# Optimization experiments

Hardware: AMD Instinct MI355X
Metric: run time of the kernel (lower is better)

## Reference

```python
import jax, jax.numpy as jnp
import numpy as np

N = 100000      # nodes
E = 800000      # edges
F_IN = 128      # input feature dim
HID = 8         # per-head hidden
HEADS = 8
HD = HID * HEADS  # 64
G = 128         # graphs in batch
C = 10          # classes
SLOPE = 0.2     # leaky relu negative slope


def setup_inputs() -> dict:
    key = jax.random.key(0)
    ks = iter(jax.random.split(key, 48))
    def rn(shape, scale=0.1):
        return jax.random.normal(next(ks), shape, jnp.float32) * scale
    inp = {
        'x': jax.random.normal(next(ks), (N, F_IN), jnp.float32),
        'edge_index': jax.random.randint(next(ks), (2, E), 0, N),
        'batch': jnp.sort(jax.random.randint(next(ks), (N,), 0, G)),
        # GAT layer 1
        'W1': rn((F_IN, HEADS * HID)), 'as1': rn((HEADS, HID)), 'ad1': rn((HEADS, HID)), 'b1': jnp.zeros((HEADS * HID,), jnp.float32),
        # GAT layer 2
        'W2': rn((HD, HEADS * HID)), 'as2': rn((HEADS, HID)), 'ad2': rn((HEADS, HID)), 'b2': jnp.zeros((HEADS * HID,), jnp.float32),
        # node attention MLP (HD -> HD//2 -> 2)
        'na_w1': rn((HD, HD // 2)), 'na_b1': jnp.zeros((HD // 2,), jnp.float32), 'na_w2': rn((HD // 2, 2)), 'na_b2': jnp.zeros((2,), jnp.float32),
        # edge attention MLP (2*HD -> HD -> 2)
        'ea_w1': rn((2 * HD, HD)), 'ea_b1': jnp.zeros((HD,), jnp.float32), 'ea_w2': rn((HD, 2)), 'ea_b2': jnp.zeros((2,), jnp.float32),
        # GCN causal / trivial
        'gc_w': rn((HD, HD)), 'gc_b': jnp.zeros((HD,), jnp.float32),
        'gt_w': rn((HD, HD)), 'gt_b': jnp.zeros((HD,), jnp.float32),
        # readouts
        'rc_w': rn((HD, HD)), 'rc_b': jnp.zeros((HD,), jnp.float32),
        'rt_w': rn((HD, HD)), 'rt_b': jnp.zeros((HD,), jnp.float32),
        # classifiers (HD -> HD//2 -> C), combined (2HD -> HD -> C)
        'cc_w1': rn((HD, HD // 2)), 'cc_b1': jnp.zeros((HD // 2,), jnp.float32), 'cc_w2': rn((HD // 2, C)), 'cc_b2': jnp.zeros((C,), jnp.float32),
        'ct_w1': rn((HD, HD // 2)), 'ct_b1': jnp.zeros((HD // 2,), jnp.float32), 'ct_w2': rn((HD // 2, C)), 'ct_b2': jnp.zeros((C,), jnp.float32),
        'cm_w1': rn((2 * HD, HD)), 'cm_b1': jnp.zeros((HD,), jnp.float32), 'cm_w2': rn((HD, C)), 'cm_b2': jnp.zeros((C,), jnp.float32),
    }
    return inp


def _mlp2(h, w1, b1, w2, b2):
    return jax.nn.relu(h @ w1 + b1) @ w2 + b2


def reference(x, edge_index, batch,
              W1, as1, ad1, b1, W2, as2, ad2, b2,
              na_w1, na_b1, na_w2, na_b2,
              ea_w1, ea_b1, ea_w2, ea_b2,
              gc_w, gc_b, gt_w, gt_b,
              rc_w, rc_b, rt_w, rt_b,
              cc_w1, cc_b1, cc_w2, cc_b2,
              ct_w1, ct_b1, ct_w2, ct_b2,
              cm_w1, cm_b1, cm_w2, cm_b2):
    src, dst = edge_index[0], edge_index[1]
    loop = jnp.arange(N)
    s2 = jnp.concatenate([src, loop])  # edges + self-loops (PyG GATConv/GCNConv add self-loops)
    d2 = jnp.concatenate([dst, loop])

    def gat(h_in, W, a_s, a_d, b):
        h = (h_in @ W).reshape(N, HEADS, HID)
        es = jnp.einsum('nhd,hd->nh', h, a_s)
        ed = jnp.einsum('nhd,hd->nh', h, a_d)
        logit = jax.nn.leaky_relu(es[s2] + ed[d2], SLOPE)      # [E+N, H]
        m = jax.ops.segment_max(logit, d2, num_segments=N)
        ex = jnp.exp(logit - m[d2])
        den = jax.ops.segment_sum(ex, d2, num_segments=N)
        alpha = ex / (den[d2] + 1e-16)
        out = jax.ops.segment_sum(h[s2] * alpha[..., None], d2, num_segments=N)
        return out.reshape(N, HEADS * HID) + b

    # GNN encoder (dropout disabled: eval mode)
    H1 = jax.nn.elu(gat(x, W1, as1, ad1, b1))
    H = gat(H1, W2, as2, ad2, b2)                              # [N, HD]

    # node attention
    na = jax.nn.softmax(_mlp2(H, na_w1, na_b1, na_w2, na_b2), axis=1)
    alpha_c, alpha_t = na[:, 0], na[:, 1]
    # edge attention (original edges, no self-loops)
    ef = jnp.concatenate([H[src], H[dst]], axis=1)             # [E, 2*HD]
    ea = jax.nn.softmax(_mlp2(ef, ea_w1, ea_b1, ea_w2, ea_b2), axis=1)
    beta_c, beta_t = ea[:, 0], ea[:, 1]

    Hc = H * alpha_c[:, None]
    Ht = H * alpha_t[:, None]

    def gcn(h_in, w, b, ew):
        # PyG gcn_norm: self-loops with weight 1, symmetric deg^-1/2 normalization
        w_full = jnp.concatenate([ew, jnp.ones((N,), h_in.dtype)])
        deg = jax.ops.segment_sum(w_full, d2, num_segments=N)
        dis = jnp.where(deg > 0, jax.lax.rsqrt(jnp.maximum(deg, 1e-20)), 0.0)
        norm = dis[s2] * w_full * dis[d2]
        h = h_in @ w
        return jax.ops.segment_sum(h[s2] * norm[:, None], d2, num_segments=N) + b

    Gc = gcn(Hc, gc_w, gc_b, beta_c)
    Gt = gcn(Ht, gt_w, gt_b, beta_t)

    # readout: linear then global_add_pool
    hGc = jax.ops.segment_sum(Gc @ rc_w + rc_b, batch, num_segments=G)  # [G, HD]
    hGt = jax.ops.segment_sum(Gt @ rt_w + rt_b, batch, num_segments=G)

    zc = _mlp2(hGc, cc_w1, cc_b1, cc_w2, cc_b2)
    zt = _mlp2(hGt, ct_w1, ct_b1, ct_w2, ct_b2)
    # RandomIntervention: within-graph node shuffle followed by add-pool == plain add-pool
    h_comb = jnp.concatenate([hGc + hGt], axis=1) if False else (hGc + hGt)
    zp = _mlp2(jnp.concatenate([h_comb, jnp.zeros_like(h_comb)], axis=1), cm_w1, cm_b1, cm_w2, cm_b2) if False else _mlp2_comb(h_comb, cm_w1, cm_b1, cm_w2, cm_b2)
    return (zc, zt, zp, hGc, hGt)


def _mlp2_comb(h_comb, cm_w1, cm_b1, cm_w2, cm_b2):
    # original: classifier_combined takes hidden_dim*2 input; forward feeds h_G_c + shuffled_h_G_t
    # which is [G, HD]; to match Linear(2*HD, ...) we use the first HD rows of cm_w1 twice?
    # NO -- the original code as written passes a [G, HD] tensor to a Linear(2*HD, HD) layer,
    # which would error in torch. Faithful runnable interpretation: combined feature is
    # concat([h_G_c, shuffled_h_G_t]) of width 2*HD (the standard CAL formulation).
    return jax.nn.relu(h_comb @ cm_w1 + cm_b1) @ cm_w2 + cm_b2


# clean final definition overriding the commented exploration above
def reference(x, edge_index, batch,
              W1, as1, ad1, b1, W2, as2, ad2, b2,
              na_w1, na_b1, na_w2, na_b2,
              ea_w1, ea_b1, ea_w2, ea_b2,
              gc_w, gc_b, gt_w, gt_b,
              rc_w, rc_b, rt_w, rt_b,
              cc_w1, cc_b1, cc_w2, cc_b2,
              ct_w1, ct_b1, ct_w2, ct_b2,
              cm_w1, cm_b1, cm_w2, cm_b2):
    src, dst = edge_index[0], edge_index[1]
    loop = jnp.arange(N)
    s2 = jnp.concatenate([src, loop])
    d2 = jnp.concatenate([dst, loop])

    def gat(h_in, W, a_s, a_d, b):
        h = (h_in @ W).reshape(N, HEADS, HID)
        es = jnp.einsum('nhd,hd->nh', h, a_s)
        ed = jnp.einsum('nhd,hd->nh', h, a_d)
        logit = jax.nn.leaky_relu(es[s2] + ed[d2], SLOPE)
        m = jax.ops.segment_max(logit, d2, num_segments=N)
        ex = jnp.exp(logit - m[d2])
        den = jax.ops.segment_sum(ex, d2, num_segments=N)
        alpha = ex / (den[d2] + 1e-16)
        out = jax.ops.segment_sum(h[s2] * alpha[..., None], d2, num_segments=N)
        return out.reshape(N, HEADS * HID) + b

    H1 = jax.nn.elu(gat(x, W1, as1, ad1, b1))
    H = gat(H1, W2, as2, ad2, b2)

    na = jax.nn.softmax(_mlp2(H, na_w1, na_b1, na_w2, na_b2), axis=1)
    alpha_c, alpha_t = na[:, 0], na[:, 1]
    ef = jnp.concatenate([H[src], H[dst]], axis=1)
    ea = jax.nn.softmax(_mlp2(ef, ea_w1, ea_b1, ea_w2, ea_b2), axis=1)
    beta_c, beta_t = ea[:, 0], ea[:, 1]

    Hc = H * alpha_c[:, None]
    Ht = H * alpha_t[:, None]

    def gcn(h_in, w, b, ew):
        w_full = jnp.concatenate([ew, jnp.ones((N,), h_in.dtype)])
        deg = jax.ops.segment_sum(w_full, d2, num_segments=N)
        dis = jnp.where(deg > 0, jax.lax.rsqrt(jnp.maximum(deg, 1e-20)), 0.0)
        norm = dis[s2] * w_full * dis[d2]
        h = h_in @ w
        return jax.ops.segment_sum(h[s2] * norm[:, None], d2, num_segments=N) + b

    Gc = gcn(Hc, gc_w, gc_b, beta_c)
    Gt = gcn(Ht, gt_w, gt_b, beta_t)

    hGc = jax.ops.segment_sum(Gc @ rc_w + rc_b, batch, num_segments=G)
    hGt = jax.ops.segment_sum(Gt @ rt_w + rt_b, batch, num_segments=G)

    zc = _mlp2(hGc, cc_w1, cc_b1, cc_w2, cc_b2)
    zt = _mlp2(hGt, ct_w1, ct_b1, ct_w2, ct_b2)
    # RandomIntervention with sorted batch: within-graph permutation + add-pool == add-pool
    h_comb = jnp.concatenate([hGc, hGt], axis=1)  # [G, 2*HD] for Linear(2*HD, ...)
    zp = _mlp2(h_comb, cm_w1, cm_b1, cm_w2, cm_b2)
    return (zc, zt, zp, hGc, hGt)


if __name__ == '__main__':
    out = reference(**setup_inputs())
    print([o.shape for o in out])
```

## Files before the change

kernel.cpp:

```cpp
#include <hip/hip_runtime.h>
#include <hip/hip_bf16.h>

#define N_NODES 100000
#define E_EDGES 800000
#define E2 (E_EDGES + N_NODES)
#define FIN 128
#define HD 64
#define NH 8
#define NG 128
#define NC 10
#define SLOPE 0.2f
#define SELF_FLAG 0x40000000
#define SRC_MASK  0x3FFFFFFF
#define NSCAN_BLK 391
#define NBLK64 1563
#define GB 16

#define U1_STRIPES 261
#define U1_GRID (2 + U1_STRIPES * 7)
#define U1_HISTB (U1_STRIPES * 4)
#define T1 (U1_STRIPES * 3)
#define U2_STRIPES 391
#define U2_GRID (U2_STRIPES * 11)

typedef unsigned short bfu;

__device__ __forceinline__ float lrelu(float x) { return x > 0.f ? x : SLOPE * x; }

__device__ __forceinline__ bfu f2bf(float f) {
    unsigned int u = __float_as_uint(f);
    u += 0x7FFFu + ((u >> 16) & 1u);
    return (bfu)(u >> 16);
}
__device__ __forceinline__ float bf2f(bfu s) {
    return __uint_as_float(((unsigned int)s) << 16);
}
__device__ __forceinline__ float bflo(unsigned int u) { return __uint_as_float(u << 16); }
__device__ __forceinline__ float bfhi(unsigned int u) { return __uint_as_float(u & 0xFFFF0000u); }

template<typename TIN, int KIN, int MODE>
__device__ __forceinline__
void gemm_tile_body(float* smem, int tile,
                    const TIN* __restrict__ in, const float* __restrict__ W,
                    bfu* __restrict__ outB,
                    const float* __restrict__ a_s, const float* __restrict__ a_d,
                    float* __restrict__ es, float* __restrict__ ed)
{
    constexpr int KH = (KIN > 64) ? 64 : KIN;
    constexpr int RS = KIN + 4;
    float* Ws   = smem;
    float* rows = smem + KH * 64;
    int t = threadIdx.x;
    int base = tile * 64;

    if constexpr (sizeof(TIN) == 4) {
        constexpr int RQ = KIN / 4;
        for (int i = t; i < 64 * RQ; i += 256) {
            int r = i / RQ, c = (i % RQ) * 4;
            int n = base + r;
            float4 v = make_float4(0.f, 0.f, 0.f, 0.f);
            if (n < N_NODES) v = *(const float4*)((const float*)in + (size_t)n * KIN + c);
            *(float4*)(rows + r * RS + c) = v;
        }
    } else {
        constexpr int RQ = KIN / 8;
        for (int i = t; i < 64 * RQ; i += 256) {
            int r = i / RQ, c = (i % RQ) * 8;
            int n = base + r;
            uint4 v = make_uint4(0, 0, 0, 0);
            if (n < N_NODES) v = *(const uint4*)((const bfu*)in + (size_t)n * KIN + c);
            float* dp = rows + r * RS + c;
            *(float4*)dp       = make_float4(bflo(v.x), bfhi(v.x), bflo(v.y), bfhi(v.y));
            *(float4*)(dp + 4) = make_float4(bflo(v.z), bfhi(v.z), bflo(v.w), bfhi(v.w));
        }
    }

    int tr = t >> 4, tc = t & 15;
    float acc[4][4] = {};
    const float4* R4 = (const float4*)rows;

    for (int h = 0; h < KIN / KH; ++h) {
        __syncthreads();
        {
            const float4* Wv = (const float4*)(W + (size_t)h * KH * 64);
            float4* Wsv4 = (float4*)Ws;
            for (int i = t; i < KH * 16; i += 256) Wsv4[i] = Wv[i];
        }
        __syncthreads();
        const float4* Wsv = (const float4*)Ws;
#pragma unroll 2
        for (int k = 0; k < KH; k += 4) {
            float4 w0 = Wsv[(k + 0) * 16 + tc];
            float4 w1 = Wsv[(k + 1) * 16 + tc];
            float4 w2 = Wsv[(k + 2) * 16 + tc];
            float4 w3 = Wsv[(k + 3) * 16 + tc];
            int kq = (h * KH + k) >> 2;
#pragma unroll
            for (int i = 0; i < 4; ++i) {
                float4 r = R4[(tr * 4 + i) * (RS / 4) + kq];
                acc[i][0] = fmaf(r.x, w0.x, fmaf(r.y, w1.x, fmaf(r.z, w2.x, fmaf(r.w, w3.x, acc[i][0]))));
                acc[i][1] = fmaf(r.x, w0.y, fmaf(r.y, w1.y, fmaf(r.z, w2.y, fmaf(r.w, w3.y, acc[i][1]))));
                acc[i][2] = fmaf(r.x, w0.z, fmaf(r.y, w1.z, fmaf(r.z, w2.z, fmaf(r.w, w3.z, acc[i][2]))));
                acc[i][3] = fmaf(r.x, w0.w, fmaf(r.y, w1.w, fmaf(r.z, w2.w, fmaf(r.w, w3.w, acc[i][3]))));
            }
        }
    }

    int j0 = tc * 4;
#pragma unroll
    for (int i = 0; i < 4; ++i) {
        int n = base + tr * 4 + i;
        if (n < N_NODES) {
            ushort4 ov;
            ov.x = f2bf(acc[i][0]); ov.y = f2bf(acc[i][1]);
            ov.z = f2bf(acc[i][2]); ov.w = f2bf(acc[i][3]);
            *(ushort4*)(outB + (size_t)n * 64 + j0) = ov;
        }
    }
    if (MODE == 1) {
        float s0[4], s1[4];
#pragma unroll
        for (int i = 0; i < 4; ++i) {
            float pes = 0.f, ped = 0.f;
#pragma unroll
            for (int q = 0; q < 4; ++q) {
                pes = fmaf(acc[i][q], a_s[j0 + q], pes);
                ped = fmaf(acc[i][q], a_d[j0 + q], ped);
            }
            pes += __shfl_xor(pes, 1, 64);
            ped += __shfl_xor(ped, 1, 64);
            s0[i] = pes; s1[i] = ped;
        }
        if ((tc & 1) == 0) {
            int h = tc >> 1;
#pragma unroll
            for (int i = 0; i < 4; ++i) {
                int n = base + tr * 4 + i;
                if (n < N_NODES) {
                    es[n * NH + h] = s0[i];
                    ed[n * NH + h] = s1[i];
                }
            }
        }
    }
}

__device__ __forceinline__
void gemm_dual_body(float* smem, int tile,
                    const bfu* __restrict__ in, const float* __restrict__ W0,
                    const float* __restrict__ W1,
                    bfu* __restrict__ out0, bfu* __restrict__ out1)
{
    float* Ws   = smem;
    float* rows = smem + 8192;
    int t = threadIdx.x;
    int base = tile * 64;
    {
        const float4* W0v = (const float4*)W0;
        const float4* W1v = (const float4*)W1;
        float4* Wsv = (float4*)Ws;
        for (int i = t; i < 1024; i += 256) { Wsv[i] = W0v[i]; Wsv[1024 + i] = W1v[i]; }
    }
    for (int i = t; i < 64 * 8; i += 256) {
        int r = i >> 3, c = (i & 7) * 8;
        int n = base + r;
        uint4 v = make_uint4(0, 0, 0, 0);
        if (n < N_NODES) v = *(const uint4*)(in + (size_t)n * 64 + c);
        float* dp = rows + r * 68 + c;
        *(float4*)dp       = make_float4(bflo(v.x), bfhi(v.x), bflo(v.y), bfhi(v.y));
        *(float4*)(dp + 4) = make_float4(bflo(v.z), bfhi(v.z), bflo(v.w), bfhi(v.w));
    }
    __syncthreads();
    int tr = t >> 4, tc = t & 15;
    float a0[4][4] = {}, a1[4][4] = {};
    const float4* Wsv = (const float4*)Ws;
    const float4* R4 = (const float4*)rows;
#pragma unroll 2
    for (int k = 0; k < 64; k += 4) {
        float4 p0 = Wsv[(k + 0) * 16 + tc];
        float4 p1 = Wsv[(k + 1) * 16 + tc];
        float4 p2 = Wsv[(k + 2) * 16 + tc];
        float4 p3 = Wsv[(k + 3) * 16 + tc];
        float4 q0 = Wsv[1024 + (k + 0) * 16 + tc];
        float4 q1 = Wsv[1024 + (k + 1) * 16 + tc];
        float4 q2 = Wsv[1024 + (k + 2) * 16 + tc];
        float4 q3 = Wsv[1024 + (k + 3) * 16 + tc];
        int kq = k >> 2;
#pragma unroll
        for (int i = 0; i < 4; ++i) {
            float4 r = R4[(tr * 4 + i) * 17 + kq];
            a0[i][0] = fmaf(r.x, p0.x, fmaf(r.y, p1.x, fmaf(r.z, p2.x, fmaf(r.w, p3.x, a0[i][0]))));
            a0[i][1] = fmaf(r.x, p0.y, fmaf(r.y, p1.y, fmaf(r.z, p2.y, fmaf(r.w, p3.y, a0[i][1]))));
            a0[i][2] = fmaf(r.x, p0.z, fmaf(r.y, p1.z, fmaf(r.z, p2.z, fmaf(r.w, p3.z, a0[i][2]))));
            a0[i][3] = fmaf(r.x, p0.w, fmaf(r.y, p1.w, fmaf(r.z, p2.w, fmaf(r.w, p3.w, a0[i][3]))));
            a1[i][0] = fmaf(r.x, q0.x, fmaf(r.y, q1.x, fmaf(r.z, q2.x, fmaf(r.w, q3.x, a1[i][0]))));
            a1[i][1] = fmaf(r.x, q0.y, fmaf(r.y, q1.y, fmaf(r.z, q2.y, fmaf(r.w, q3.y, a1[i][1]))));
            a1[i][2] = fmaf(r.x, q0.z, fmaf(r.y, q1.z, fmaf(r.z, q2.z, fmaf(r.w, q3.z, a1[i][2]))));
            a1[i][3] = fmaf(r.x, q0.w, fmaf(r.y, q1.w, fmaf(r.z, q2.w, fmaf(r.w, q3.w, a1[i][3]))));
        }
    }
    int j0 = tc * 4;
#pragma unroll
    for (int i = 0; i < 4; ++i) {
        int n = base + tr * 4 + i;
        if (n >= N_NODES) continue;
        ushort4 o0, o1;
        o0.x = f2bf(a0[i][0]); o0.y = f2bf(a0[i][1]);
        o0.z = f2bf(a0[i][2]); o0.w = f2bf(a0[i][3]);
        o1.x = f2bf(a1[i][0]); o1.y = f2bf(a1[i][1]);
        o1.z = f2bf(a1[i][2]); o1.w = f2bf(a1[i][3]);
        *(ushort4*)(out0 + (size_t)n * 64 + j0) = o0;
        *(ushort4*)(out1 + (size_t)n * 64 + j0) = o1;
    }
}

__device__ __forceinline__
void node_att_body(float* smem, int tile,
                   const bfu* __restrict__ H, const float* __restrict__ w1,
                   const float* __restrict__ b1, const float* __restrict__ w2,
                   const float* __restrict__ b2, float2* __restrict__ al2)
{
    float* w1s  = smem;
    float* w2s  = smem + 2048;
    float* rows = smem + 2112;
    int t = threadIdx.x;
    int base = tile * 64;
    {
        const float4* w1v = (const float4*)w1;
        float4* dst = (float4*)w1s;
        for (int i = t; i < 512; i += 256) dst[i] = w1v[i];
    }
    if (t < 64) w2s[t] = w2[t];
    for (int i = t; i < 64 * 8; i += 256) {
        int r = i >> 3, c = (i & 7) * 8;
        int n = base + r;
        uint4 v = make_uint4(0, 0, 0, 0);
        if (n < N_NODES) v = *(const uint4*)(H + (size_t)n * 64 + c);
        float* dp = rows + r * 65 + c;
        dp[0] = bflo(v.x); dp[1] = bfhi(v.x);
        dp[2] = bflo(v.y); dp[3] = bfhi(v.y);
        dp[4] = bflo(v.z); dp[5] = bfhi(v.z);
        dp[6] = bflo(v.w); dp[7] = bfhi(v.w);
    }
    __syncthreads();
    int tr = t >> 3;
    int tc = t & 7;
    float4 bv = *(const float4*)(b1 + tc * 4);
    float4 acc0 = bv, acc1 = bv;
    const float4* w1sv = (const float4*)w1s;
#pragma unroll 8
    for (int k = 0; k < 64; ++k) {
        float4 w = w1sv[k * 8 + tc];
        float r0 = rows[tr * 65 + k];
        float r1 = rows[(tr + 32) * 65 + k];
        acc0.x = fmaf(r0, w.x, acc0.x); acc0.y = fmaf(r0, w.y, acc0.y);
        acc0.z = fmaf(r0, w.z, acc0.z); acc0.w = fmaf(r0, w.w, acc0.w);
        acc1.x = fmaf(r1, w.x, acc1.x); acc1.y = fmaf(r1, w.y, acc1.y);
        acc1.z = fmaf(r1, w.z, acc1.z); acc1.w = fmaf(r1, w.w, acc1.w);
    }
    float z00 = 0.f, z01 = 0.f, z10 = 0.f, z11 = 0.f;
    float h0, w20, w21;
    int j0 = tc * 4;
#pragma unroll
    for (int q = 0; q < 4; ++q) {
        float a0q = q == 0 ? acc0.x : q == 1 ? acc0.y : q == 2 ? acc0.z : acc0.w;
        float a1q = q == 0 ? acc1.x : q == 1 ? acc1.y : q == 2 ? acc1.z : acc1.w;
        w20 = w2s[(j0 + q) * 2]; w21 = w2s[(j0 + q) * 2 + 1];
        h0 = fmaxf(a0q, 0.f);
        z00 = fmaf(h0, w20, z00); z01 = fmaf(h0, w21, z01);
        h0 = fmaxf(a1q, 0.f);
        z10 = fmaf(h0, w20, z10); z11 = fmaf(h0, w21, z11);
    }
#pragma unroll
    for (int o = 1; o < 8; o <<= 1) {
        z00 += __shfl_xor(z00, o, 64); z01 += __shfl_xor(z01, o, 64);
        z10 += __shfl_xor(z10, o, 64); z11 += __shfl_xor(z11, o, 64);
    }
    if (tc == 0) {
        int n0 = base + tr, n1 = base + tr + 32;
        if (n0 < N_NODES) {
            float zz0 = z00 + b2[0], zz1 = z01 + b2[1];
            float mx = fmaxf(zz0, zz1);
            float e0 = __expf(zz0 - mx), e1 = __expf(zz1 - mx);
            float ss = e0 + e1;
            al2[n0] = make_float2(e0 / ss, e1 / ss);
        }
        if (n1 < N_NODES) {
            float zz0 = z10 + b2[0], zz1 = z11 + b2[1];
            float mx = fmaxf(zz0, zz1);
            float e0 = __expf(zz0 - mx), e1 = __expf(zz1 - mx);
            float ss = e0 + e1;
            al2[n1] = make_float2(e0 / ss, e1 / ss);
        }
    }
}

__device__ __forceinline__
void weight_prep_body(float* smem,
                      const float* __restrict__ gw, const float* __restrict__ gb,
                      const float* __restrict__ rw, const float* __restrict__ rb,
                      float* __restrict__ Wp, float* __restrict__ bp)
{
    float* A = smem;
    float* B = smem + 4096;
    int t = threadIdx.x;
    {
        const float4* ga = (const float4*)gw;
        const float4* rA = (const float4*)rw;
        float4* dA = (float4*)A; float4* dB = (float4*)B;
        for (int i = t; i < 1024; i += 256) { dA[i] = ga[i]; dB[i] = rA[i]; }
    }
    __syncthreads();
    for (int e = t * 16; e < t * 16 + 16; ++e) {
        int k = e >> 6, j = e & 63;
        float acc = 0.f;
#pragma unroll 8
        for (int m = 0; m < 64; ++m) acc = fmaf(A[k * 64 + m], B[m * 64 + j], acc);
        Wp[e] = acc;
    }
    if (t < 64) {
        float acc = rb[t];
#pragma unroll 8
        for (int m = 0; m < 64; ++m) acc = fmaf(gb[m], B[m * 64 + t], acc);
        bp[t] = acc;
    }
}

__global__ __launch_bounds__(256)
void u1_fused(const float* __restrict__ x, const float* __restrict__ W1,
              bfu* __restrict__ B0, const float* __restrict__ as1,
              const float* __restrict__ ad1, float* __restrict__ es,
              float* __restrict__ ed,
              const int* __restrict__ ei, int* __restrict__ cnt,
              int* __restrict__ rank,
              const float* __restrict__ gc_w, const float* __restrict__ gc_b,
              const float* __restrict__ rc_w, const float* __restrict__ rc_b,
              const float* __restrict__ gt_w, const float* __restrict__ gt_b,
              const float* __restrict__ rt_w, const float* __restrict__ rt_b,
              float* __restrict__ Wcp, float* __restrict__ bcp,
              float* __restrict__ Wtp, float* __restrict__ btp)
{
    __shared__ __align__(16) float smem[12544];
    int b = blockIdx.x;
    if (b < 2) {
        if (b == 0) weight_prep_body(smem, gc_w, gc_b, rc_w, rc_b, Wcp, bcp);
        else        weight_prep_body(smem, gt_w, gt_b, rt_w, rt_b, Wtp, btp);
        return;
    }
    int u = b - 2;
    int stripe = u / 7, r = u % 7;
    if (r < 3) {
        gemm_tile_body<float, FIN, 1>(smem, stripe * 3 + r, x, W1, B0, as1, ad1, es, ed);
    } else {
        int idx = stripe * 4 + (r - 3);
        int t = threadIdx.x;
        for (int e = idx * 256 + t; e < E_EDGES; e += U1_HISTB * 256) {
            int d = ei[E_EDGES + e];
            rank[e] = atomicAdd(&cnt[d], 1);
        }
    }
}

__global__ __launch_bounds__(256)
void u2_fused(const float* __restrict__ x, const float* __restrict__ W1,
              bfu* __restrict__ B0, const float* __restrict__ as1,
              const float* __restrict__ ad1, float* __restrict__ es,
              float* __restrict__ ed,
              const int* __restrict__ ei, const int* __restrict__ rank,
              const int* __restrict__ offs,
              int* __restrict__ csr, int* __restrict__ csrd)
{
    __shared__ __align__(16) float smem[12544];
    int b = blockIdx.x;
    int stripe = b / 11, r = b % 11;
    int t = threadIdx.x;
    if (r < 8) {
        int e = (stripe * 8 + r) * 256 + t;
        if (e < E_EDGES) {
            int s = ei[e], d = ei[E_EDGES + e];
            csr[offs[d] + rank[e]] = s;
        }
    } else if (r < 10) {
        int tile = T1 + stripe * 2 + (r - 8);
        if (tile < NBLK64)
            gemm_tile_body<float, FIN, 1>(smem, tile, x, W1, B0, as1, ad1, es, ed);
    } else {
        int n = stripe * 256 + t;
        if (n < N_NODES) {
            int pb = offs[n], pe = offs[n + 1];
            for (int p = pb; p < pe; ++p) csrd[p] = n;
            csr[pe - 1] = n | SELF_FLAG;
        }
    }
}

__global__ __launch_bounds__(256)
void u3_fused(const bfu* __restrict__ B2,
              const float* __restrict__ na_w1, const float* __restrict__ na_b1,
              const float* __restrict__ na_w2, const float* __restrict__ na_b2,
              float2* __restrict__ al2,
              const float* __restrict__ ea_w1,
              bfu* __restrict__ P1, bfu* __restrict__ P2)
{
    __shared__ __align__(16) float smem[12544];
    int b = blockIdx.x;
    if (b & 1) node_att_body(smem, b >> 1, B2, na_w1, na_b1, na_w2, na_b2, al2);
    else       gemm_dual_body(smem, b >> 1, B2, ea_w1, ea_w1 + 64 * 64, P1, P2);
}

__global__ __launch_bounds__(256)
void gemm_tile_k64(const bfu* __restrict__ in, const float* __restrict__ W,
                   bfu* __restrict__ outB,
                   const float* __restrict__ a_s, const float* __restrict__ a_d,
                   float* __restrict__ es, float* __restrict__ ed)
{
    __shared__ __align__(16) float smem[64 * 64 + 64 * 68];
    gemm_tile_body<bfu, 64, 1>(smem, blockIdx.x, in, W, outB, a_s, a_d, es, ed);
}

__global__ void csr_scan1(const int* __restrict__ cnt, int* __restrict__ offs,
                          int* __restrict__ bsum)
{
    __shared__ int tmp[256];
    int t = threadIdx.x;
    int i = blockIdx.x * 256 + t;
    int v = (i < N_NODES) ? cnt[i] + 1 : 0;
    tmp[t] = v; __syncthreads();
#pragma unroll
    for (int o = 1; o < 256; o <<= 1) {
        int a = (t >= o) ? tmp[t - o] : 0;
        __syncthreads();
        tmp[t] += a;
        __syncthreads();
    }
    if (i < N_NODES) offs[i] = tmp[t] - v;
    if (t == 255) bsum[blockIdx.x] = tmp[255];
}

__global__ void csr_scan2(int* __restrict__ bsum)
{
    __shared__ int tmp[512];
    int t = threadIdx.x;
    int v = (t < NSCAN_BLK) ? bsum[t] : 0;
    tmp[t] = v; __syncthreads();
#pragma unroll
    for (int o = 1; o < 512; o <<= 1) {
        int a = (t >= o) ? tmp[t - o] : 0;
        __syncthreads();
        tmp[t] += a;
        __syncthreads();
    }
    if (t < NSCAN_BLK) bsum[t] = tmp[t] - v;
}

__global__ void csr_scan3(int* __restrict__ offs, const int* __restrict__ bsum)
{
    int i = blockIdx.x * 256 + threadIdx.x;
    if (i < N_NODES) offs[i] += bsum[blockIdx.x];
    if (i == 0) offs[N_NODES] = E2;
}

template<int ELU>
__global__ void gat_aggregate4(const int* __restrict__ offs, const int* __restrict__ csr,
                               const float* __restrict__ es, const float* __restrict__ ed,
                               const bfu* __restrict__ hsrcB, const float* __restrict__ bias,
                               bfu* __restrict__ outB)
{
    int n = blockIdx.x * 4 + (threadIdx.x >> 6);
    int lane = threadIdx.x & 63;
    if (n >= N_NODES) return;
    int g  = lane >> 4;
    int fl = lane & 15;
    int h  = fl >> 1;
    int beg = offs[n], end = offs[n + 1];
    float edv = ed[n * NH + h];
    float den = 0.f;
    float4 acc = make_float4(0.f, 0.f, 0.f, 0.f);
    int p = beg + g;
    for (; p + 4 < end; p += 8) {
        int s0 = csr[p] & SRC_MASK;
        int s1 = csr[p + 4] & SRC_MASK;
        float l0 = lrelu(es[s0 * NH + h] + edv);
        float l1 = lrelu(es[s1 * NH + h] + edv);
        float ex0 = __expf(l0);
        float ex1 = __expf(l1);
        den += ex0 + ex1;
        ushort4 ra = *(const ushort4*)(hsrcB + (size_t)s0 * HD + fl * 4);
        ushort4 rb = *(const ushort4*)(hsrcB + (size_t)s1 * HD + fl * 4);
        acc.x = fmaf(bf2f(ra.x), ex0, fmaf(bf2f(rb.x), ex1, acc.x));
        acc.y = fmaf(bf2f(ra.y), ex0, fmaf(bf2f(rb.y), ex1, acc.y));
        acc.z = fmaf(bf2f(ra.z), ex0, fmaf(bf2f(rb.z), ex1, acc.z));
        acc.w = fmaf(bf2f(ra.w), ex0, fmaf(bf2f(rb.w), ex1, acc.w));
    }
    if (p < end) {
        int s = csr[p] & SRC_MASK;
        float l = lrelu(es[s * NH + h] + edv);
        float ex = __expf(l);
        den += ex;
        ushort4 rb = *(const ushort4*)(hsrcB + (size_t)s * HD + fl * 4);
        acc.x = fmaf(bf2f(rb.x), ex, acc.x);
        acc.y = fmaf(bf2f(rb.y), ex, acc.y);
        acc.z = fmaf(bf2f(rb.z), ex, acc.z);
        acc.w = fmaf(bf2f(rb.w), ex, acc.w);
    }
#pragma unroll
    for (int o = 16; o <= 32; o <<= 1) {
        den   += __shfl_xor(den,   o, 64);
        acc.x += __shfl_xor(acc.x, o, 64);
        acc.y += __shfl_xor(acc.y, o, 64);
        acc.z += __shfl_xor(acc.z, o, 64);
        acc.w += __shfl_xor(acc.w, o, 64);
    }
    if (g == 0) {
        float inv = 1.f / (den + 1e-16f);
        float4 bv = *(const float4*)(bias + fl * 4);
        float v0 = acc.x * inv + bv.x;
        float v1 = acc.y * inv + bv.y;
        float v2 = acc.z * inv + bv.z;
        float v3 = acc.w * inv + bv.w;
        if (ELU) {
            v0 = v0 > 0.f ? v0 : (__expf(v0) - 1.f);
            v1 = v1 > 0.f ? v1 : (__expf(v1) - 1.f);
            v2 = v2 > 0.f ? v2 : (__expf(v2) - 1.f);
            v3 = v3 > 0.f ? v3 : (__expf(v3) - 1.f);
        }
        ushort4 ov;
        ov.x = f2bf(v0); ov.y = f2bf(v1); ov.z = f2bf(v2); ov.w = f2bf(v3);
        *(ushort4*)(outB + (size_t)n * HD + fl * 4) = ov;
    }
}

__global__ void edge_att_node(const int* __restrict__ offs, const int* __restrict__ csr,
                              const bfu* __restrict__ P1b, const bfu* __restrict__ P2b,
                              const float* __restrict__ b1, const float* __restrict__ w2,
                              const float* __restrict__ b2,
                              const float2* __restrict__ al2,
                              float2* __restrict__ beta2, float2* __restrict__ dis2,
                              float2* __restrict__ prod2)
{
    int n = blockIdx.x * 4 + (threadIdx.x >> 6);
    int lane = threadIdx.x & 63;
    if (n >= N_NODES) return;
    int slot = lane >> 3, q = lane & 7;
    uint4 U2 = *(const uint4*)(P2b + (size_t)n * 64 + q * 8);
    const float4* pb = (const float4*)(b1 + q * 8);
    const float4* pw = (const float4*)(w2 + q * 16);
    float4 c0 = pb[0], c1 = pb[1];
    float4 w0 = pw[0], w1v = pw[1], w2v = pw[2], w3v = pw[3];
    float wd0 = w0.x - w0.y,   wd1 = w0.z - w0.w;
    float wd2 = w1v.x - w1v.y, wd3 = w1v.z - w1v.w;
    float wd4 = w2v.x - w2v.y, wd5 = w2v.z - w2v.w;
    float wd6 = w3v.x - w3v.y, wd7 = w3v.z - w3v.w;
    float zbd = b2[0] - b2[1];
    float d0 = bflo(U2.x) + c0.x, d1 = bfhi(U2.x) + c0.y;
    float d2 = bflo(U2.y) + c0.z, d3 = bfhi(U2.y) + c0.w;
    float d4 = bflo(U2.z) + c1.x, d5 = bfhi(U2.z) + c1.y;
    float d6 = bflo(U2.w) + c1.z, d7 = bfhi(U2.w) + c1.w;
    int beg = offs[n], end = offs[n + 1];
    float dc = 0.f, dt = 0.f;
    for (int p = beg + slot; p < end; p += 8) {
        int sv = csr[p];
        if (sv & SELF_FLAG) {
            if (q == 0) { dc += 1.f; dt += 1.f; }
            continue;
        }
        uint4 U1 = *(const uint4*)(P1b + (size_t)sv * 64 + q * 8);
        float h0 = fmaxf(bflo(U1.x) + d0, 0.f);
        float h1 = fmaxf(bfhi(U1.x) + d1, 0.f);
        float h2 = fmaxf(bflo(U1.y) + d2, 0.f);
        float h3 = fmaxf(bfhi(U1.y) + d3, 0.f);
        float h4 = fmaxf(bflo(U1.z) + d4, 0.f);
        float h5 = fmaxf(bfhi(U1.z) + d5, 0.f);
        float h6 = fmaxf(bflo(U1.w) + d6, 0.f);
        float h7 = fmaxf(bfhi(U1.w) + d7, 0.f);
        float z = fmaf(h0, wd0, fmaf(h1, wd1, fmaf(h2, wd2, fmaf(h3, wd3,
                  fmaf(h4, wd4, fmaf(h5, wd5, fmaf(h6, wd6, h7 * wd7)))))));
        z += __shfl_xor(z, 1, 64);
        z += __shfl_xor(z, 2, 64);
        z += __shfl_xor(z, 4, 64);
        if (q == 0) {
            z += zbd;
            float e = __expf(-fabsf(z));
            float inv = 1.f / (1.f + e);
            float bx = z >= 0.f ? inv : e * inv;
            float by = z >= 0.f ? e * inv : inv;
            beta2[p] = make_float2(bx, by);
            dc += bx; dt += by;
        }
    }
    dc += __shfl_xor(dc, 8, 64);  dt += __shfl_xor(dt, 8, 64);
    dc += __shfl_xor(dc, 16, 64); dt += __shfl_xor(dt, 16, 64);
    dc += __shfl_xor(dc, 32, 64); dt += __shfl_xor(dt, 32, 64);
    if (lane == 0) {
        float ic = rsqrtf(fmaxf(dc, 1e-20f));
        float it = rsqrtf(fmaxf(dt, 1e-20f));
        dis2[n] = make_float2(ic, it);
        float2 al = al2[n];
        prod2[n] = make_float2(ic * al.x, it * al.y);
    }
}

__global__ __launch_bounds__(256)
void gcn_readout_fused(const int* __restrict__ offs, const int* __restrict__ csr,
                       const int* __restrict__ csrd, const int* __restrict__ batch,
                       const bfu* __restrict__ HB,
                       const float2* __restrict__ beta2, const float2* __restrict__ dis2,
                       const float2* __restrict__ prod2,
                       float* __restrict__ Pc, float* __restrict__ Pt)
{
    int g = blockIdx.x / GB, b = blockIdx.x % GB;
    int t = threadIdx.x;
    int lo, hi;
    {
        int l = 0, r = N_NODES;
        while (l < r) { int m = (l + r) >> 1; if (batch[m] < g) l = m + 1; else r = m; }
        lo = l;
        r = N_NODES;
        while (l < r) { int m = (l + r) >> 1; if (batch[m] < g + 1) l = m + 1; else r = m; }
        hi = l;
    }
    int pbeg = offs[lo], pend = offs[hi];
    int total = pend - pbeg;
    int chunk = (total + GB - 1) / GB;
    int start = pbeg + b * chunk;
    int end = start + chunk;
    if (end > pend) end = pend;
    if (start > pend) start = pend;
    int slot = t >> 4, fl = t & 15;
    float4 a1 = make_float4(0.f, 0.f, 0.f, 0.f);
    float4 a2 = make_float4(0.f, 0.f, 0.f, 0.f);
    int p = start + slot;
    for (; p + 48 < end; p += 64) {
#pragma unroll
        for (int j = 0; j < 4; ++j) {
            int pp = p + j * 16;
            int sv = csr[pp];
            int s = sv & SRC_MASK;
            float2 bb = beta2[pp];
            if (sv & SELF_FLAG) { bb.x = 1.f; bb.y = 1.f; }
            float2 pr = prod2[s];
            float2 dv = dis2[csrd[pp]];
            float wc = pr.x * bb.x * dv.x;
            float wt = pr.y * bb.y * dv.y;
            ushort4 r0 = *(const ushort4*)(HB + (size_t)s * HD + fl * 4);
            float f0 = bf2f(r0.x), f1 = bf2f(r0.y), f2 = bf2f(r0.z), f3 = bf2f(r0.w);
            a1.x = fmaf(f0, wc, a1.x); a1.y = fmaf(f1, wc, a1.y);
            a1.z = fmaf(f2, wc, a1.z); a1.w = fmaf(f3, wc, a1.w);
            a2.x = fmaf(f0, wt, a2.x); a2.y = fmaf(f1, wt, a2.y);
            a2.z = fmaf(f2, wt, a2.z); a2.w = fmaf(f3, wt, a2.w);
        }
    }
    for (; p < end; p += 16) {
        int sv = csr[p];
        int s = sv & SRC_MASK;
        float2 bb = beta2[p];
        if (sv & SELF_FLAG) { bb.x = 1.f; bb.y = 1.f; }
        float2 pr = prod2[s];
        float2 dv = dis2[csrd[p]];
        float wc = pr.x * bb.x * dv.x;
        float wt = pr.y * bb.y * dv.y;
        ushort4 r0 = *(const ushort4*)(HB + (size_t)s * HD + fl * 4);
        float f0 = bf2f(r0.x), f1 = bf2f(r0.y), f2 = bf2f(r0.z), f3 = bf2f(r0.w);
        a1.x = fmaf(f0, wc, a1.x); a1.y = fmaf(f1, wc, a1.y);
        a1.z = fmaf(f2, wc, a1.z); a1.w = fmaf(f3, wc, a1.w);
        a2.x = fmaf(f0, wt, a2.x); a2.y = fmaf(f1, wt, a2.y);
        a2.z = fmaf(f2, wt, a2.z); a2.w = fmaf(f3, wt, a2.w);
    }
    __shared__ float redc[16 * 64], redt[16 * 64];
    *(float4*)(redc + slot * 64 + fl * 4) = a1;
    *(float4*)(redt + slot * 64 + fl * 4) = a2;
    __syncthreads();
    if (t < 64) {
        float sc = 0.f, st = 0.f;
#pragma unroll
        for (int s = 0; s < 16; ++s) { sc += redc[s * 64 + t]; st += redt[s * 64 + t]; }
        Pc[(size_t)blockIdx.x * 64 + t] = sc;
        Pt[(size_t)blockIdx.x * 64 + t] = st;
    }
}

__global__ __launch_bounds__(64)
void head_final(const float* __restrict__ Pc, const float* __restrict__ Pt,
                const int* __restrict__ batch,
                const float* __restrict__ Wcp, const float* __restrict__ bcp,
                const float* __restrict__ Wtp, const float* __restrict__ btp,
                const float* __restrict__ cc_w1, const float* __restrict__ cc_b1,
                const float* __restrict__ cc_w2, const float* __restrict__ cc_b2,
                const float* __restrict__ ct_w1, const float* __restrict__ ct_b1,
                const float* __restrict__ ct_w2, const float* __restrict__ ct_b2,
                const float* __restrict__ cm_w1, const float* __restrict__ cm_b1,
                const float* __restrict__ cm_w2, const float* __restrict__ cm_b2,
                float* __restrict__ out)
{
    int g = blockIdx.x;
    int t = threadIdx.x;
    __shared__ float scl[64], stl[64], hgc[64], hgt[64], hid[64];
    float sc = 0.f, st = 0.f;
#pragma unroll
    for (int b = 0; b < GB; ++b) {
        sc += Pc[(size_t)(g * GB + b) * 64 + t];
        st += Pt[(size_t)(g * GB + b) * 64 + t];
    }
    scl[t] = sc; stl[t] = st;
    int lo, hi;
    {
        int l = 0, r = N_NODES;
        while (l < r) { int m = (l + r) >> 1; if (batch[m] < g) l = m + 1; else r = m; }
        lo = l;
        r = N_NODES;
        while (l < r) { int m = (l + r) >> 1; if (batch[m] < g + 1) l = m + 1; else r = m; }
        hi = l;
    }
    float c = (float)(hi - lo);
    __syncthreads();
    {
        float a = c * bcp[t], bb = c * btp[t];
#pragma unroll 8
        for (int k = 0; k < 64; ++k) {
            a  = fmaf(scl[k], Wcp[k * 64 + t], a);
            bb = fmaf(stl[k], Wtp[k * 64 + t], bb);
        }
        hgc[t] = a; hgt[t] = bb;
        out[3840 + g * 64 + t]  = a;
        out[12032 + g * 64 + t] = bb;
    }
    __syncthreads();
    if (t < 32) {
        float a = cc_b1[t];
#pragma unroll 8
        for (int k = 0; k < 64; ++k) a = fmaf(hgc[k], cc_w1[k * 32 + t], a);
        hid[t] = fmaxf(a, 0.f);
    }
    __syncthreads();
    if (t < NC) {
        float a = cc_b2[t];
#pragma unroll
        for (int k = 0; k < 32; ++k) a = fmaf(hid[k], cc_w2[k * NC + t], a);
        out[g * NC + t] = a;
    }
    __syncthreads();
    if (t < 32) {
        float a = ct_b1[t];
#pragma unroll 8
        for (int k = 0; k < 64; ++k) a = fmaf(hgt[k], ct_w1[k * 32 + t], a);
        hid[t] = fmaxf(a, 0.f);
    }
    __syncthreads();
    if (t < NC) {
        float a = ct_b2[t];
#pragma unroll
        for (int k = 0; k < 32; ++k) a = fmaf(hid[k], ct_w2[k * NC + t], a);
        out[1280 + g * NC + t] = a;
    }
    __syncthreads();
    {
        float a = cm_b1[t];
#pragma unroll 8
        for (int k = 0; k < 64; ++k) {
            a = fmaf(hgc[k], cm_w1[k * 64 + t], a);
            a = fmaf(hgt[k], cm_w1[(64 + k) * 64 + t], a);
        }
        hid[t] = fmaxf(a, 0.f);
    }
    __syncthreads();
    if (t < NC) {
        float a = cm_b2[t];
#pragma unroll 8
        for (int k = 0; k < 64; ++k) a = fmaf(hid[k], cm_w2[k * NC + t], a);
        out[2560 + g * NC + t] = a;
    }
}

extern "C" void kernel_launch(void* const* d_in, const int* in_sizes, int n_in,
                              void* d_out, int out_size, void* d_ws, size_t ws_size,
                              hipStream_t stream)
{
    const float* x     = (const float*)d_in[0];
    const int*   ei    = (const int*)d_in[1];
    const int*   batch = (const int*)d_in[2];
    const float* W1    = (const float*)d_in[3];
    const float* as1   = (const float*)d_in[4];
    const float* ad1   = (const float*)d_in[5];
    const float* b1    = (const float*)d_in[6];
    const float* W2    = (const float*)d_in[7];
    const float* as2   = (const float*)d_in[8];
    const float* ad2   = (const float*)d_in[9];
    const float* b2    = (const float*)d_in[10];
    const float* na_w1 = (const float*)d_in[11];
    const float* na_b1 = (const float*)d_in[12];
    const float* na_w2 = (const float*)d_in[13];
    const float* na_b2 = (const float*)d_in[14];
    const float* ea_w1 = (const float*)d_in[15];
    const float* ea_b1 = (const float*)d_in[16];
    const float* ea_w2 = (const float*)d_in[17];
    const float* ea_b2 = (const float*)d_in[18];
    const float* gc_w  = (const float*)d_in[19];
    const float* gc_b  = (const float*)d_in[20];
    const float* gt_w  = (const float*)d_in[21];
    const float* gt_b  = (const float*)d_in[22];
    const float* rc_w  = (const float*)d_in[23];
    const float* rc_b  = (const float*)d_in[24];
    const float* rt_w  = (const float*)d_in[25];
    const float* rt_b  = (const float*)d_in[26];
    const float* cc_w1 = (const float*)d_in[27];
    const float* cc_b1 = (const float*)d_in[28];
    const float* cc_w2 = (const float*)d_in[29];
    const float* cc_b2 = (const float*)d_in[30];
    const float* ct_w1 = (const float*)d_in[31];
    const float* ct_b1 = (const float*)d_in[32];
    const float* ct_w2 = (const float*)d_in[33];
    const float* ct_b2 = (const float*)d_in[34];
    const float* cm_w1 = (const float*)d_in[35];
    const float* cm_b1 = (const float*)d_in[36];
    const float* cm_w2 = (const float*)d_in[37];
    const float* cm_b2 = (const float*)d_in[38];
    float* out = (float*)d_out;

    float* ws = (float*)d_ws;
    size_t o = 0;
    const size_t nf = (size_t)N_NODES * HD;
    float* es    = ws + o; o += (size_t)N_NODES * NH;
    float* ed    = ws + o; o += (size_t)N_NODES * NH;
    float2* al2  = (float2*)(ws + o); o += (size_t)N_NODES * 2;
    float2* beta2= (float2*)(ws + o); o += (size_t)E2 * 2;
    float2* dis2 = (float2*)(ws + o); o += (size_t)N_NODES * 2;
    float2* prod2= (float2*)(ws + o); o += (size_t)N_NODES * 2;
    bfu* B0      = (bfu*)(ws + o); o += nf / 2;
    bfu* B1      = (bfu*)(ws + o); o += nf / 2;
    bfu* B2      = (bfu*)(ws + o); o += nf / 2;
    bfu* BH1     = (bfu*)(ws + o); o += nf / 2;
    int* csr     = (int*)(ws + o); o += E2;
    int* csrd    = (int*)(ws + o); o += E2;
    int* offs    = (int*)(ws + o); o += N_NODES + 1;
    float* Pc    = ws + o; o += (size_t)NG * GB * 64;
    float* Pt    = ws + o; o += (size_t)NG * GB * 64;
    float* Wcp   = ws + o; o += 4096;
    float* Wtp   = ws + o; o += 4096;
    float* bcp   = ws + o; o += 64;
    float* btp   = ws + o; o += 64;
    int* cnt  = (int*)beta2;
    int* bsum = (int*)dis2;
    int* rank = (int*)B1;

    const int NW_BLKS = N_NODES / 4;

    hipMemsetAsync(cnt, 0, (size_t)N_NODES * 4, stream);
    u1_fused<<<U1_GRID, 256, 0, stream>>>(x, W1, B0, as1, ad1, es, ed,
                                          ei, cnt, rank,
                                          gc_w, gc_b, rc_w, rc_b,
                                          gt_w, gt_b, rt_w, rt_b,
                                          Wcp, bcp, Wtp, btp);
    csr_scan1<<<NSCAN_BLK, 256, 0, stream>>>(cnt, offs, bsum);
    csr_scan2<<<1, 512, 0, stream>>>(bsum);
    csr_scan3<<<NSCAN_BLK, 256, 0, stream>>>(offs, bsum);

    u2_fused<<<U2_GRID, 256, 0, stream>>>(x, W1, B0, as1, ad1, es, ed,
                                          ei, rank, offs, csr, csrd);

    gat_aggregate4<1><<<NW_BLKS, 256, 0, stream>>>(offs, csr, es, ed, B0, b1, BH1);

    gemm_tile_k64<<<NBLK64, 256, 0, stream>>>(BH1, W2, B0, as2, ad2, es, ed);
    gat_aggregate4<0><<<NW_BLKS, 256, 0, stream>>>(offs, csr, es, ed, B0, b2, B2);

    u3_fused<<<2 * NBLK64, 256, 0, stream>>>(B2, na_w1, na_b1, na_w2, na_b2, al2,
                                             ea_w1, B0, B1);

    edge_att_node<<<NW_BLKS, 256, 0, stream>>>(offs, csr, B0, B1,
                                               ea_b1, ea_w2, ea_b2, al2,
                                               beta2, dis2, prod2);

    gcn_readout_fused<<<NG * GB, 256, 0, stream>>>(offs, csr, csrd, batch, B2,
                                                   beta2, dis2, prod2, Pc, Pt);

    head_final<<<NG, 64, 0, stream>>>(Pc, Pt, batch,
                                      Wcp, bcp, Wtp, btp,
                                      cc_w1, cc_b1, cc_w2, cc_b2,
                                      ct_w1, ct_b1, ct_w2, ct_b2,
                                      cm_w1, cm_b1, cm_w2, cm_b2, out);
    (void)in_sizes; (void)n_in; (void)out_size; (void)ws_size;
}
```

Baseline: 493.7 us.

## Merge CSR scan passes, precompute graph bounds, drop self-loop branch in edge attention

Merges the second and third CSR scan kernels into one, where each block sums the preceding block totals itself, removing a kernel launch. Graph boundaries in the sorted batch vector are found once by binary search in the first scan kernel and reused by the readout and head kernels instead of being searched per block. The edge-attention kernel assumes the self-loop is the last CSR entry per node, skips it in the loop and adds its contribution afterwards, which removes a per-edge branch. The histogram loop is also unrolled by two to overlap atomics, at the cost of relying on the self-loop placement invariant.

Result: faster. 479.2 us (-2.9%).

```diff
diff --git a/kernel.cpp b/kernel.cpp
--- a/kernel.cpp
+++ b/kernel.cpp
@@ -354,9 +354,16 @@
     } else {
         int idx = stripe * 4 + (r - 3);
         int t = threadIdx.x;
-        for (int e = idx * 256 + t; e < E_EDGES; e += U1_HISTB * 256) {
-            int d = ei[E_EDGES + e];
-            rank[e] = atomicAdd(&cnt[d], 1);
+        const int STR = U1_HISTB * 256;
+        for (int e = idx * 256 + t; e < E_EDGES; e += 2 * STR) {
+            int e1 = e + STR;
+            int d0 = ei[E_EDGES + e];
+            int r0 = atomicAdd(&cnt[d0], 1);
+            int r1 = 0;
+            bool has1 = e1 < E_EDGES;
+            if (has1) r1 = atomicAdd(&cnt[ei[E_EDGES + e1]], 1);
+            rank[e] = r0;
+            if (has1) rank[e1] = r1;
         }
     }
 }
@@ -419,7 +426,8 @@
 }
 
 __global__ void csr_scan1(const int* __restrict__ cnt, int* __restrict__ offs,
-                          int* __restrict__ bsum)
+                          int* __restrict__ bsum, const int* __restrict__ batch,
+                          int* __restrict__ glo)
 {
     __shared__ int tmp[256];
     int t = threadIdx.x;
@@ -435,28 +443,29 @@
     }
     if (i < N_NODES) offs[i] = tmp[t] - v;
     if (t == 255) bsum[blockIdx.x] = tmp[255];
-}
-
-__global__ void csr_scan2(int* __restrict__ bsum)
-{
-    __shared__ int tmp[512];
+    if (blockIdx.x == 0 && t <= NG) {
+        int l = 0, r = N_NODES;
+        while (l < r) { int m = (l + r) >> 1; if (batch[m] < t) l = m + 1; else r = m; }
+        glo[t] = l;
+    }
+}
+
+__global__ void csr_scan23(int* __restrict__ offs, const int* __restrict__ bsum)
+{
+    __shared__ int tmp[256];
+    int b = blockIdx.x;
     int t = threadIdx.x;
-    int v = (t < NSCAN_BLK) ? bsum[t] : 0;
-    tmp[t] = v; __syncthreads();
-#pragma unroll
-    for (int o = 1; o < 512; o <<= 1) {
-        int a = (t >= o) ? tmp[t - o] : 0;
+    int s = 0;
+    for (int j = t; j < b; j += 256) s += bsum[j];
+    tmp[t] = s; __syncthreads();
+#pragma unroll
+    for (int o = 128; o > 0; o >>= 1) {
+        if (t < o) tmp[t] += tmp[t + o];
         __syncthreads();
-        tmp[t] += a;
-        __syncthreads();
-    }
-    if (t < NSCAN_BLK) bsum[t] = tmp[t] - v;
-}
-
-__global__ void csr_scan3(int* __restrict__ offs, const int* __restrict__ bsum)
-{
-    int i = blockIdx.x * 256 + threadIdx.x;
-    if (i < N_NODES) offs[i] += bsum[blockIdx.x];
+    }
+    int prefix = tmp[0];
+    int i = b * 256 + t;
+    if (i < N_NODES) offs[i] += prefix;
     if (i == 0) offs[N_NODES] = E2;
 }
 
@@ -556,15 +565,11 @@
     float d2 = bflo(U2.y) + c0.z, d3 = bfhi(U2.y) + c0.w;
     float d4 = bflo(U2.z) + c1.x, d5 = bfhi(U2.z) + c1.y;
     float d6 = bflo(U2.w) + c1.z, d7 = bfhi(U2.w) + c1.w;
-    int beg = offs[n], end = offs[n + 1];
+    int beg = offs[n], endr = offs[n + 1] - 1;
     float dc = 0.f, dt = 0.f;
-    for (int p = beg + slot; p < end; p += 8) {
-        int sv = csr[p];
-        if (sv & SELF_FLAG) {
-            if (q == 0) { dc += 1.f; dt += 1.f; }
-            continue;
-        }
-        uint4 U1 = *(const uint4*)(P1b + (size_t)sv * 64 + q * 8);
+    for (int p = beg + slot; p < endr; p += 8) {
+        int s = csr[p];
+        uint4 U1 = *(const uint4*)(P1b + (size_t)s * 64 + q * 8);
         float h0 = fmaxf(bflo(U1.x) + d0, 0.f);
         float h1 = fmaxf(bfhi(U1.x) + d1, 0.f);
         float h2 = fmaxf(bflo(U1.y) + d2, 0.f);
@@ -592,6 +597,7 @@
     dc += __shfl_xor(dc, 16, 64); dt += __shfl_xor(dt, 16, 64);
     dc += __shfl_xor(dc, 32, 64); dt += __shfl_xor(dt, 32, 64);
     if (lane == 0) {
+        dc += 1.f; dt += 1.f;
         float ic = rsqrtf(fmaxf(dc, 1e-20f));
         float it = rsqrtf(fmaxf(dt, 1e-20f));
         dis2[n] = make_float2(ic, it);
@@ -602,7 +608,7 @@
 
 __global__ __launch_bounds__(256)
 void gcn_readout_fused(const int* __restrict__ offs, const int* __restrict__ csr,
-                       const int* __restrict__ csrd, const int* __restrict__ batch,
+                       const int* __restrict__ csrd, const int* __restrict__ glo,
                        const bfu* __restrict__ HB,
                        const float2* __restrict__ beta2, const float2* __restrict__ dis2,
                        const float2* __restrict__ prod2,
@@ -610,16 +616,7 @@
 {
     int g = blockIdx.x / GB, b = blockIdx.x % GB;
     int t = threadIdx.x;
-    int lo, hi;
-    {
-        int l = 0, r = N_NODES;
-        while (l < r) { int m = (l + r) >> 1; if (batch[m] < g) l = m + 1; else r = m; }
-        lo = l;
-        r = N_NODES;
-        while (l < r) { int m = (l + r) >> 1; if (batch[m] < g + 1) l = m + 1; else r = m; }
-        hi = l;
-    }
-    int pbeg = offs[lo], pend = offs[hi];
+    int pbeg = offs[glo[g]], pend = offs[glo[g + 1]];
     int total = pend - pbeg;
     int chunk = (total + GB - 1) / GB;
     int start = pbeg + b * chunk;
@@ -681,7 +678,7 @@
 
 __global__ __launch_bounds__(64)
 void head_final(const float* __restrict__ Pc, const float* __restrict__ Pt,
-                const int* __restrict__ batch,
+                const int* __restrict__ glo,
                 const float* __restrict__ Wcp, const float* __restrict__ bcp,
                 const float* __restrict__ Wtp, const float* __restrict__ btp,
                 const float* __restrict__ cc_w1, const float* __restrict__ cc_b1,
@@ -702,16 +699,7 @@
         st += Pt[(size_t)(g * GB + b) * 64 + t];
     }
     scl[t] = sc; stl[t] = st;
-    int lo, hi;
-    {
-        int l = 0, r = N_NODES;
-        while (l < r) { int m = (l + r) >> 1; if (batch[m] < g) l = m + 1; else r = m; }
-        lo = l;
-        r = N_NODES;
-        while (l < r) { int m = (l + r) >> 1; if (batch[m] < g + 1) l = m + 1; else r = m; }
-        hi = l;
-    }
-    float c = (float)(hi - lo);
+    float c = (float)(glo[g + 1] - glo[g]);
     __syncthreads();
     {
         float a = c * bcp[t], bb = c * btp[t];
@@ -838,6 +826,7 @@
     float* Wtp   = ws + o; o += 4096;
     float* bcp   = ws + o; o += 64;
     float* btp   = ws + o; o += 64;
+    int* glo     = (int*)(ws + o); o += NG + 2;
     int* cnt  = (int*)beta2;
     int* bsum = (int*)dis2;
     int* rank = (int*)B1;
@@ -850,9 +839,8 @@
                                           gc_w, gc_b, rc_w, rc_b,
                                           gt_w, gt_b, rt_w, rt_b,
                                           Wcp, bcp, Wtp, btp);
-    csr_scan1<<<NSCAN_BLK, 256, 0, stream>>>(cnt, offs, bsum);
-    csr_scan2<<<1, 512, 0, stream>>>(bsum);
-    csr_scan3<<<NSCAN_BLK, 256, 0, stream>>>(offs, bsum);
+    csr_scan1<<<NSCAN_BLK, 256, 0, stream>>>(cnt, offs, bsum, batch, glo);
+    csr_scan23<<<NSCAN_BLK, 256, 0, stream>>>(offs, bsum);
 
     u2_fused<<<U2_GRID, 256, 0, stream>>>(x, W1, B0, as1, ad1, es, ed,
                                           ei, rank, offs, csr, csrd);
@@ -869,10 +857,10 @@
                                                ea_b1, ea_w2, ea_b2, al2,
                                                beta2, dis2, prod2);
 
-    gcn_readout_fused<<<NG * GB, 256, 0, stream>>>(offs, csr, csrd, batch, B2,
+    gcn_readout_fused<<<NG * GB, 256, 0, stream>>>(offs, csr, csrd, glo, B2,
                                                    beta2, dis2, prod2, Pc, Pt);
 
-    head_final<<<NG, 64, 0, stream>>>(Pc, Pt, batch,
+    head_final<<<NG, 64, 0, stream>>>(Pc, Pt, glo,
                                       Wcp, bcp, Wtp, btp,
                                       cc_w1, cc_b1, cc_w2, cc_b2,
                                       ct_w1, ct_b1, ct_w2, ct_b2,
```
